# Optimization experiments

Hardware: AMD Instinct MI355X
Metric: run time of the kernel (lower is better)

## Reference

```python
import jax, jax.numpy as jnp
import numpy as np

PATCH_SIZE = 16
STRIDE = 16


def setup_inputs() -> dict:
    key = jax.random.key(0)
    k1, k2 = jax.random.split(key)
    x = jax.random.normal(k1, (64, 64, 8192), dtype=jnp.float32)
    mask = jax.random.randint(k2, (64, 8192), 0, 2, dtype=jnp.int32)
    return {"x": x, "mask": mask}


def reference(x, mask):
    B, C, S = x.shape
    P, St = PATCH_SIZE, STRIDE
    n_patches = 1 + (S - P) // St
    # window gather indices: [n_patches, P]
    idx = jnp.arange(n_patches)[:, None] * St + jnp.arange(P)[None, :]
    # x[:, :, idx] -> [B, C, n_patches, P]; torch stacks on dim=1 -> [B, n_patches, C, P]
    patches = jnp.transpose(x[:, :, idx], (0, 2, 1, 3)).reshape(B, n_patches, C * P)
    # per-patch valid ratio over the window, thresholded at 0.5 -> float mask [B, n_patches]
    valid_ratio = jnp.mean(mask[:, idx].astype(jnp.float32), axis=-1)
    padding_mask = (valid_ratio >= 0.5).astype(jnp.float32)
    return patches, padding_mask
```

## Files before the change

kernel.cpp:

```cpp
#include <hip/hip_runtime.h>


constexpr int Bb  = 64;
constexpr int Cc  = 64;
constexpr int Ss  = 8192;
constexpr int NP  = 512;
constexpr int PT  = 8;
constexpr int ROWF = PT * 16;
constexpr int LSTRIDE = ROWF + 4;
constexpr size_t PATCH_ELEMS = (size_t)Bb * NP * Cc * 16;

__global__ __launch_bounds__(256) void ts_patcher_kernel(
    const float* __restrict__ x,
    const int*   __restrict__ mask,
    float*       __restrict__ out)
{
    __shared__ float lds[Cc * LSTRIDE];

    const int t   = threadIdx.x;
    const int blk = blockIdx.x;
    const int b   = blk >> 6;
    const int P0  = (blk & 63) * PT;

    const float* xb = x + (size_t)b * Cc * Ss + P0 * 16;

    {
        const int c0  = t >> 5;
        const int col = (t & 31) * 4;
#pragma unroll
        for (int i = 0; i < 8; ++i) {
            const int c = i * 8 + c0;
            const float4 v = *(const float4*)(xb + (size_t)c * Ss + col);
            *(float4*)(&lds[c * LSTRIDE + col]) = v;
        }
    }

    __syncthreads();

    {
        float* otile = out + ((size_t)(b * NP + P0) * (Cc * 16));
        const int c = t >> 2;
        const int j = (t & 3) * 4;
#pragma unroll
        for (int i = 0; i < 8; ++i) {
            const float4 v = *(const float4*)(&lds[c * LSTRIDE + i * 16 + j]);
            *(float4*)(otile + (size_t)i * 1024 + t * 4) = v;
        }
    }

    if (t < PT) {
        const int p = P0 + t;
        const int4* m = (const int4*)(mask + (size_t)b * Ss + p * 16);
        int4 a = m[0], d = m[1], e = m[2], f = m[3];
        int s = a.x + a.y + a.z + a.w
              + d.x + d.y + d.z + d.w
              + e.x + e.y + e.z + e.w
              + f.x + f.y + f.z + f.w;
        out[PATCH_ELEMS + (size_t)b * NP + p] = (s >= 8) ? 1.0f : 0.0f;
    }
}

extern "C" void kernel_launch(void* const* d_in, const int* in_sizes, int n_in,
                              void* d_out, int out_size, void* d_ws, size_t ws_size,
                              hipStream_t stream) {
    const float* x    = (const float*)d_in[0];
    const int*   mask = (const int*)d_in[1];
    float*       out  = (float*)d_out;

    const int blocks = Bb * (NP / PT);
    ts_patcher_kernel<<<blocks, 256, 0, stream>>>(x, mask, out);
}
```

Before: 228.9 us.

## Drop LDS transpose; map blocks per channel row with strided direct stores

Reassigns each block to a single (batch, channel) row so reads are fully contiguous. Each thread writes its float4 chunks directly to the strided output positions, removing the shared-memory staging and the barrier. Mask reduction moves to the channel-0 block, with each thread handling two patches. This trades coalesced 4KB row writes for 64-byte scattered writes, which may stress write combining.

```diff
diff --git a/kernel.cpp b/kernel.cpp
--- a/kernel.cpp
+++ b/kernel.cpp
@@ -1,13 +1,12 @@
 #include <hip/hip_runtime.h>
 
+
+typedef float f4 __attribute__((ext_vector_type(4)));
 
 constexpr int Bb  = 64;
 constexpr int Cc  = 64;
 constexpr int Ss  = 8192;
 constexpr int NP  = 512;
-constexpr int PT  = 8;
-constexpr int ROWF = PT * 16;
-constexpr int LSTRIDE = ROWF + 4;
 constexpr size_t PATCH_ELEMS = (size_t)Bb * NP * Cc * 16;
 
 __global__ __launch_bounds__(256) void ts_patcher_kernel(
@@ -15,48 +14,39 @@
     const int*   __restrict__ mask,
     float*       __restrict__ out)
 {
-    __shared__ float lds[Cc * LSTRIDE];
-
     const int t   = threadIdx.x;
     const int blk = blockIdx.x;
     const int b   = blk >> 6;
-    const int P0  = (blk & 63) * PT;
+    const int c   = blk & 63;
 
-    const float* xb = x + (size_t)b * Cc * Ss + P0 * 16;
+    const float* xr = x + ((size_t)b * Cc + c) * Ss;
 
-    {
-        const int c0  = t >> 5;
-        const int col = (t & 31) * 4;
+    f4* ob = (f4*)out + (size_t)b * 131072 + (size_t)c * 4;
+
+    f4 v[8];
 #pragma unroll
-        for (int i = 0; i < 8; ++i) {
-            const int c = i * 8 + c0;
-            const float4 v = *(const float4*)(xb + (size_t)c * Ss + col);
-            *(float4*)(&lds[c * LSTRIDE + col]) = v;
-        }
+    for (int i = 0; i < 8; ++i)
+        v[i] = *(const f4*)(xr + (size_t)i * 1024 + t * 4);
+
+#pragma unroll
+    for (int i = 0; i < 8; ++i) {
+        const int p = i * 64 + (t >> 2);
+        ob[(size_t)p * 256 + (t & 3)] = v[i];
     }
 
-    __syncthreads();
-
-    {
-        float* otile = out + ((size_t)(b * NP + P0) * (Cc * 16));
-        const int c = t >> 2;
-        const int j = (t & 3) * 4;
+    if (c == 0) {
+        const int4* mb = (const int4*)(mask + (size_t)b * Ss);
 #pragma unroll
-        for (int i = 0; i < 8; ++i) {
-            const float4 v = *(const float4*)(&lds[c * LSTRIDE + i * 16 + j]);
-            *(float4*)(otile + (size_t)i * 1024 + t * 4) = v;
+        for (int k = 0; k < 2; ++k) {
+            const int p = 2 * t + k;
+            int4 a = mb[p * 4 + 0], d = mb[p * 4 + 1];
+            int4 e = mb[p * 4 + 2], f = mb[p * 4 + 3];
+            int s = a.x + a.y + a.z + a.w
+                  + d.x + d.y + d.z + d.w
+                  + e.x + e.y + e.z + e.w
+                  + f.x + f.y + f.z + f.w;
+            out[PATCH_ELEMS + (size_t)b * NP + p] = (s >= 8) ? 1.0f : 0.0f;
         }
-    }
-
-    if (t < PT) {
-        const int p = P0 + t;
-        const int4* m = (const int4*)(mask + (size_t)b * Ss + p * 16);
-        int4 a = m[0], d = m[1], e = m[2], f = m[3];
-        int s = a.x + a.y + a.z + a.w
-              + d.x + d.y + d.z + d.w
-              + e.x + e.y + e.z + e.w
-              + f.x + f.y + f.z + f.w;
-        out[PATCH_ELEMS + (size_t)b * NP + p] = (s >= 8) ? 1.0f : 0.0f;
     }
 }
 
@@ -67,6 +57,6 @@
     const int*   mask = (const int*)d_in[1];
     float*       out  = (float*)d_out;
 
-    const int blocks = Bb * (NP / PT);
+    const int blocks = Bb * Cc;
     ts_patcher_kernel<<<blocks, 256, 0, stream>>>(x, mask, out);
 }
```

Result: slower. 254.3 us (+11.1%).
